# Kernel optimization log

Measured on AMD Instinct MI355X. Metric: run time of the kernel, lower is better.

Reference implementation:

```python
import jax, jax.numpy as jnp
import numpy as np

ALPHA = 16.0
RANK = 64
SCALING = ALPHA / RANK


def setup_inputs() -> dict:
    key = jax.random.key(0)
    k1, k2, k3, k4, k5 = jax.random.split(key, 5)
    B, S, DIN, DOUT = 4, 4096, 4096, 4096
    x = jax.random.normal(k1, (B, S, DIN), dtype=jnp.float32)
    lora_A = jax.random.normal(k2, (RANK, DIN), dtype=jnp.float32) / np.sqrt(DIN)
    lora_B = jax.random.normal(k3, (DOUT, RANK), dtype=jnp.float32)
    lora_A_scale = jax.random.uniform(k4, (RANK,), dtype=jnp.float32, minval=0.5, maxval=1.5)
    lora_B_scale = jax.random.uniform(k5, (DOUT,), dtype=jnp.float32, minval=0.5, maxval=1.5)
    return {"x": x, "lora_A": lora_A, "lora_B": lora_B,
            "lora_A_scale": lora_A_scale, "lora_B_scale": lora_B_scale}


def reference(x, lora_A, lora_B, lora_A_scale, lora_B_scale):
    # INT8 dequant path: quantized.float() * scale.unsqueeze(-1)
    A_dq = lora_A * lora_A_scale[:, None]          # [rank, in]
    B_dq = lora_B * lora_B_scale[:, None]          # [out, rank]
    # x @ A.T -> [B, S, rank]; then @ B.T -> [B, S, out]; final scaling
    h = jnp.einsum('bsi,ri->bsr', x, A_dq)
    out = jnp.einsum('bsr,or->bso', h, B_dq)
    return out * SCALING
```

## Files before the change

kernel.cpp:

```cpp
#include <hip/hip_runtime.h>


#define M_TOTAL 16384
#define DIN     4096
#define DOUT    4096
#define RANK    64

typedef __bf16 bf16_8 __attribute__((ext_vector_type(8)));
typedef __bf16 bf16_4 __attribute__((ext_vector_type(4)));
typedef float  f32x4  __attribute__((ext_vector_type(4)));

__global__ __launch_bounds__(256) void prep_kernel(
    const float* __restrict__ A, const float* __restrict__ Bm,
    const float* __restrict__ sA, const float* __restrict__ sB,
    __bf16* __restrict__ Abf, __bf16* __restrict__ Bbf) {
  int i = (blockIdx.x * 256 + threadIdx.x) * 4;
  float4 a = *(const float4*)(A + i);
  float sa = sA[i >> 12];
  bf16_4 va;
  va[0] = (__bf16)(a.x * sa); va[1] = (__bf16)(a.y * sa);
  va[2] = (__bf16)(a.z * sa); va[3] = (__bf16)(a.w * sa);
  *(bf16_4*)(Abf + i) = va;

  float4 b = *(const float4*)(Bm + i);
  float sb = sB[i >> 6] * 0.25f;
  bf16_4 vb;
  vb[0] = (__bf16)(b.x * sb); vb[1] = (__bf16)(b.y * sb);
  vb[2] = (__bf16)(b.z * sb); vb[3] = (__bf16)(b.w * sb);
  *(bf16_4*)(Bbf + i) = vb;
}

__global__ __launch_bounds__(256, 4) void lora_kernel(
    const float* __restrict__ x, const __bf16* __restrict__ Abf,
    const __bf16* __restrict__ Bbf, float* __restrict__ out) {
  __shared__ alignas(16) float  part[4 * 1024];
  __shared__ alignas(16) __bf16 hs[16 * RANK];

  const int t    = threadIdx.x;
  const int lane = t & 63;
  const int w    = t >> 6;
  const int lr   = lane & 15;
  const int quad = lane >> 4;
  const int mBase = blockIdx.x * 16;

  const float*  xg = x   + (size_t)(mBase + lr) * DIN + w * 1024 + quad * 8;
  const __bf16* ag = Abf + (size_t)lr * DIN           + w * 1024 + quad * 8;

  f32x4 acc0 = {0.f,0.f,0.f,0.f};
  f32x4 acc1 = {0.f,0.f,0.f,0.f};
  f32x4 acc2 = {0.f,0.f,0.f,0.f};
  f32x4 acc3 = {0.f,0.f,0.f,0.f};

  float4 f0 = *(const float4*)(xg);
  float4 f1 = *(const float4*)(xg + 4);
  bf16_8 a0 = *(const bf16_8*)(ag);
  bf16_8 a1 = *(const bf16_8*)(ag + 16 * DIN);
  bf16_8 a2 = *(const bf16_8*)(ag + 32 * DIN);
  bf16_8 a3 = *(const bf16_8*)(ag + 48 * DIN);

  for (int k = 32; k <= 1024; k += 32) {
    float4 g0 = f0, g1 = f1;
    bf16_8 c0 = a0, c1 = a1, c2 = a2, c3 = a3;
    if (k < 1024) {
      f0 = *(const float4*)(xg + k);
      f1 = *(const float4*)(xg + k + 4);
      a0 = *(const bf16_8*)(ag + k);
      a1 = *(const bf16_8*)(ag + k + 16 * DIN);
      a2 = *(const bf16_8*)(ag + k + 32 * DIN);
      a3 = *(const bf16_8*)(ag + k + 48 * DIN);
    }
    bf16_8 xv;
    xv[0] = (__bf16)g0.x; xv[1] = (__bf16)g0.y;
    xv[2] = (__bf16)g0.z; xv[3] = (__bf16)g0.w;
    xv[4] = (__bf16)g1.x; xv[5] = (__bf16)g1.y;
    xv[6] = (__bf16)g1.z; xv[7] = (__bf16)g1.w;
    acc0 = __builtin_amdgcn_mfma_f32_16x16x32_bf16(xv, c0, acc0, 0, 0, 0);
    acc1 = __builtin_amdgcn_mfma_f32_16x16x32_bf16(xv, c1, acc1, 0, 0, 0);
    acc2 = __builtin_amdgcn_mfma_f32_16x16x32_bf16(xv, c2, acc2, 0, 0, 0);
    acc3 = __builtin_amdgcn_mfma_f32_16x16x32_bf16(xv, c3, acc3, 0, 0, 0);
  }

  {
    float* pw = part + w * 1024;
#pragma unroll
    for (int i = 0; i < 4; ++i) {
      pw[(quad * 4 + i) * 64 +      lr] = acc0[i];
      pw[(quad * 4 + i) * 64 + 16 + lr] = acc1[i];
      pw[(quad * 4 + i) * 64 + 32 + lr] = acc2[i];
      pw[(quad * 4 + i) * 64 + 48 + lr] = acc3[i];
    }
  }
  __syncthreads();

  {
    const f32x4* pp = (const f32x4*)part;
    f32x4 s = pp[t] + pp[t + 256] + pp[t + 512] + pp[t + 768];
    bf16_4 hv;
    hv[0] = (__bf16)s[0]; hv[1] = (__bf16)s[1];
    hv[2] = (__bf16)s[2]; hv[3] = (__bf16)s[3];
    ((bf16_4*)hs)[t] = hv;
  }
  __syncthreads();

  bf16_8 hf0 = *(const bf16_8*)&hs[lr * RANK + quad * 8];
  bf16_8 hf1 = *(const bf16_8*)&hs[lr * RANK + 32 + quad * 8];

  const __bf16* bg = Bbf + (size_t)(w * 1024 + lr) * RANK + quad * 8;
  float* og = out + (size_t)(mBase + lr) * DOUT + w * 1024;

#pragma unroll 4
  for (int nt = 0; nt < 64; ++nt) {
    bf16_8 b0 = *(const bf16_8*)(bg + nt * 16 * RANK);
    bf16_8 b1 = *(const bf16_8*)(bg + nt * 16 * RANK + 32);
    f32x4 o = {0.f, 0.f, 0.f, 0.f};
    o = __builtin_amdgcn_mfma_f32_16x16x32_bf16(b0, hf0, o, 0, 0, 0);
    o = __builtin_amdgcn_mfma_f32_16x16x32_bf16(b1, hf1, o, 0, 0, 0);
    *(f32x4*)(og + nt * 16 + quad * 4) = o;
  }
}

extern "C" void kernel_launch(void* const* d_in, const int* in_sizes, int n_in,
                              void* d_out, int out_size, void* d_ws, size_t ws_size,
                              hipStream_t stream) {
  const float* x  = (const float*)d_in[0];
  const float* A  = (const float*)d_in[1];
  const float* Bm = (const float*)d_in[2];
  const float* sA = (const float*)d_in[3];
  const float* sB = (const float*)d_in[4];
  float* out = (float*)d_out;

  __bf16* Abf = (__bf16*)d_ws;
  __bf16* Bbf = Abf + (size_t)RANK * DIN;

  prep_kernel<<<256, 256, 0, stream>>>(A, Bm, sA, sB, Abf, Bbf);
  lora_kernel<<<M_TOTAL / 16, 256, 0, stream>>>(x, Abf, Bbf, out);
}
```

Before: 549.1 us.

## Split fused LoRA kernel into two GEMM kernels with LDS-staged loads and stores

Splits the fused kernel into two: gemm1 streams x through double-buffered LDS using global_load_lds and writes the bf16 intermediate h to workspace, and gemm2 reads h and stages output tiles in swizzled LDS so each row is written to global memory as contiguous wide stores. The aim is more efficient, coalesced traffic on the large x read and the large output write, which dominate this memory-bound workload. The cost is an extra kernel launch, a small h round-trip through memory, and lower occupancy in gemm1.

```diff
diff --git a/kernel.cpp b/kernel.cpp
--- a/kernel.cpp
+++ b/kernel.cpp
@@ -9,6 +9,10 @@
 typedef __bf16 bf16_8 __attribute__((ext_vector_type(8)));
 typedef __bf16 bf16_4 __attribute__((ext_vector_type(4)));
 typedef float  f32x4  __attribute__((ext_vector_type(4)));
+
+#define GLDS16(g, l) __builtin_amdgcn_global_load_lds( \
+    (const __attribute__((address_space(1))) void*)(g), \
+    (__attribute__((address_space(3))) void*)(l), 16, 0, 0)
 
 __global__ __launch_bounds__(256) void prep_kernel(
     const float* __restrict__ A, const float* __restrict__ Bm,
@@ -30,11 +34,94 @@
   *(bf16_4*)(Bbf + i) = vb;
 }
 
-__global__ __launch_bounds__(256, 4) void lora_kernel(
+__global__ __launch_bounds__(256, 2) void gemm1_kernel(
     const float* __restrict__ x, const __bf16* __restrict__ Abf,
-    const __bf16* __restrict__ Bbf, float* __restrict__ out) {
-  __shared__ alignas(16) float  part[4 * 1024];
-  __shared__ alignas(16) __bf16 hs[16 * RANK];
+    __bf16* __restrict__ h) {
+  __shared__ alignas(16) float xs[2][32][256];
+  __shared__ alignas(16) float part[4][16][64];
+
+  const int t    = threadIdx.x;
+  const int lane = t & 63;
+  const int w    = t >> 6;
+  const int lr   = lane & 15;
+  const int quad = lane >> 4;
+  const int mt   = w & 1;
+  const int kh   = w >> 1;
+  const int mBase = blockIdx.x * 32;
+
+  const int swz = w & 1;
+  const float* xsrc = x + (size_t)(mBase + w) * DIN + ((lane ^ swz) << 2);
+
+  const int row = mt * 16 + lr;
+  const int rs  = row & 1;
+
+  f32x4 acc0 = {0.f,0.f,0.f,0.f};
+  f32x4 acc1 = {0.f,0.f,0.f,0.f};
+  f32x4 acc2 = {0.f,0.f,0.f,0.f};
+  f32x4 acc3 = {0.f,0.f,0.f,0.f};
+
+#pragma unroll
+  for (int j = 0; j < 8; ++j)
+    GLDS16(xsrc + (size_t)j * 4 * DIN, &xs[0][w + j * 4][0]);
+  __syncthreads();
+
+  for (int s = 0; s < 16; ++s) {
+    const int buf = s & 1;
+    if (s + 1 < 16) {
+      const float* src = xsrc + (s + 1) * 256;
+#pragma unroll
+      for (int j = 0; j < 8; ++j)
+        GLDS16(src + (size_t)j * 4 * DIN, &xs[buf ^ 1][w + j * 4][0]);
+    }
+    const int k0 = s * 256;
+#pragma unroll
+    for (int ks = 0; ks < 4; ++ks) {
+      const float* px = &xs[buf][row][kh * 128 + ks * 32 + quad * 8];
+      f32x4 lo = *(const f32x4*)(px + (rs ? 4 : 0));
+      f32x4 hi = *(const f32x4*)(px + (rs ? 0 : 4));
+      bf16_8 xv;
+      xv[0]=(__bf16)lo[0]; xv[1]=(__bf16)lo[1]; xv[2]=(__bf16)lo[2]; xv[3]=(__bf16)lo[3];
+      xv[4]=(__bf16)hi[0]; xv[5]=(__bf16)hi[1]; xv[6]=(__bf16)hi[2]; xv[7]=(__bf16)hi[3];
+
+      const __bf16* ap = Abf + (size_t)lr * DIN + k0 + kh * 128 + ks * 32 + quad * 8;
+      bf16_8 a0 = *(const bf16_8*)(ap);
+      bf16_8 a1 = *(const bf16_8*)(ap + 16 * DIN);
+      bf16_8 a2 = *(const bf16_8*)(ap + 32 * DIN);
+      bf16_8 a3 = *(const bf16_8*)(ap + 48 * DIN);
+      acc0 = __builtin_amdgcn_mfma_f32_16x16x32_bf16(xv, a0, acc0, 0, 0, 0);
+      acc1 = __builtin_amdgcn_mfma_f32_16x16x32_bf16(xv, a1, acc1, 0, 0, 0);
+      acc2 = __builtin_amdgcn_mfma_f32_16x16x32_bf16(xv, a2, acc2, 0, 0, 0);
+      acc3 = __builtin_amdgcn_mfma_f32_16x16x32_bf16(xv, a3, acc3, 0, 0, 0);
+    }
+    __syncthreads();
+  }
+
+#pragma unroll
+  for (int i = 0; i < 4; ++i) {
+    part[w][quad * 4 + i][     lr] = acc0[i];
+    part[w][quad * 4 + i][16 + lr] = acc1[i];
+    part[w][quad * 4 + i][32 + lr] = acc2[i];
+    part[w][quad * 4 + i][48 + lr] = acc3[i];
+  }
+  __syncthreads();
+  {
+    int idx = t * 8;
+    int r   = idx >> 6;
+    int c   = idx & 63;
+    int m2  = r >> 4, r16 = r & 15;
+    f32x4 s0 = *(const f32x4*)&part[m2][r16][c]     + *(const f32x4*)&part[m2 + 2][r16][c];
+    f32x4 s1 = *(const f32x4*)&part[m2][r16][c + 4] + *(const f32x4*)&part[m2 + 2][r16][c + 4];
+    bf16_8 hv;
+    hv[0]=(__bf16)s0[0]; hv[1]=(__bf16)s0[1]; hv[2]=(__bf16)s0[2]; hv[3]=(__bf16)s0[3];
+    hv[4]=(__bf16)s1[0]; hv[5]=(__bf16)s1[1]; hv[6]=(__bf16)s1[2]; hv[7]=(__bf16)s1[3];
+    *(bf16_8*)(h + (size_t)(mBase + r) * RANK + c) = hv;
+  }
+}
+
+__global__ __launch_bounds__(256, 4) void gemm2_kernel(
+    const __bf16* __restrict__ h, const __bf16* __restrict__ Bbf,
+    float* __restrict__ out) {
+  __shared__ alignas(16) float os[16][512];
 
   const int t    = threadIdx.x;
   const int lane = t & 63;
@@ -43,79 +130,35 @@
   const int quad = lane >> 4;
   const int mBase = blockIdx.x * 16;
 
-  const float*  xg = x   + (size_t)(mBase + lr) * DIN + w * 1024 + quad * 8;
-  const __bf16* ag = Abf + (size_t)lr * DIN           + w * 1024 + quad * 8;
+  const __bf16* hp = h + (size_t)(mBase + lr) * RANK + quad * 8;
+  bf16_8 hf0 = *(const bf16_8*)(hp);
+  bf16_8 hf1 = *(const bf16_8*)(hp + 32);
 
-  f32x4 acc0 = {0.f,0.f,0.f,0.f};
-  f32x4 acc1 = {0.f,0.f,0.f,0.f};
-  f32x4 acc2 = {0.f,0.f,0.f,0.f};
-  f32x4 acc3 = {0.f,0.f,0.f,0.f};
-
-  float4 f0 = *(const float4*)(xg);
-  float4 f1 = *(const float4*)(xg + 4);
-  bf16_8 a0 = *(const bf16_8*)(ag);
-  bf16_8 a1 = *(const bf16_8*)(ag + 16 * DIN);
-  bf16_8 a2 = *(const bf16_8*)(ag + 32 * DIN);
-  bf16_8 a3 = *(const bf16_8*)(ag + 48 * DIN);
-
-  for (int k = 32; k <= 1024; k += 32) {
-    float4 g0 = f0, g1 = f1;
-    bf16_8 c0 = a0, c1 = a1, c2 = a2, c3 = a3;
-    if (k < 1024) {
-      f0 = *(const float4*)(xg + k);
-      f1 = *(const float4*)(xg + k + 4);
-      a0 = *(const bf16_8*)(ag + k);
-      a1 = *(const bf16_8*)(ag + k + 16 * DIN);
-      a2 = *(const bf16_8*)(ag + k + 32 * DIN);
-      a3 = *(const bf16_8*)(ag + k + 48 * DIN);
+  for (int c = 0; c < 8; ++c) {
+    const int nb = c * 512 + w * 128;
+#pragma unroll
+    for (int tt = 0; tt < 8; ++tt) {
+      const __bf16* bp = Bbf + (size_t)(nb + tt * 16 + lr) * RANK + quad * 8;
+      bf16_8 b0 = *(const bf16_8*)(bp);
+      bf16_8 b1 = *(const bf16_8*)(bp + 32);
+      f32x4 o = {0.f, 0.f, 0.f, 0.f};
+      o = __builtin_amdgcn_mfma_f32_16x16x32_bf16(b0, hf0, o, 0, 0, 0);
+      o = __builtin_amdgcn_mfma_f32_16x16x32_bf16(b1, hf1, o, 0, 0, 0);
+      int colb = (w * 128 + tt * 16 + quad * 4) * 4;
+      int addr = lr * 2048 + (colb ^ ((lr & 7) << 4));
+      *(f32x4*)((char*)os + addr) = o;
     }
-    bf16_8 xv;
-    xv[0] = (__bf16)g0.x; xv[1] = (__bf16)g0.y;
-    xv[2] = (__bf16)g0.z; xv[3] = (__bf16)g0.w;
-    xv[4] = (__bf16)g1.x; xv[5] = (__bf16)g1.y;
-    xv[6] = (__bf16)g1.z; xv[7] = (__bf16)g1.w;
-    acc0 = __builtin_amdgcn_mfma_f32_16x16x32_bf16(xv, c0, acc0, 0, 0, 0);
-    acc1 = __builtin_amdgcn_mfma_f32_16x16x32_bf16(xv, c1, acc1, 0, 0, 0);
-    acc2 = __builtin_amdgcn_mfma_f32_16x16x32_bf16(xv, c2, acc2, 0, 0, 0);
-    acc3 = __builtin_amdgcn_mfma_f32_16x16x32_bf16(xv, c3, acc3, 0, 0, 0);
-  }
-
-  {
-    float* pw = part + w * 1024;
+    __syncthreads();
 #pragma unroll
-    for (int i = 0; i < 4; ++i) {
-      pw[(quad * 4 + i) * 64 +      lr] = acc0[i];
-      pw[(quad * 4 + i) * 64 + 16 + lr] = acc1[i];
-      pw[(quad * 4 + i) * 64 + 32 + lr] = acc2[i];
-      pw[(quad * 4 + i) * 64 + 48 + lr] = acc3[i];
+    for (int r = 0; r < 8; ++r) {
+      int o4   = r * 4096 + t * 16;
+      int rr   = o4 >> 11;
+      int colb = o4 & 2047;
+      int a    = rr * 2048 + (colb ^ ((rr & 7) << 4));
+      f32x4 v  = *(const f32x4*)((const char*)os + a);
+      *(f32x4*)(out + (size_t)(mBase + rr) * DOUT + c * 512 + (colb >> 2)) = v;
     }
-  }
-  __syncthreads();
-
-  {
-    const f32x4* pp = (const f32x4*)part;
-    f32x4 s = pp[t] + pp[t + 256] + pp[t + 512] + pp[t + 768];
-    bf16_4 hv;
-    hv[0] = (__bf16)s[0]; hv[1] = (__bf16)s[1];
-    hv[2] = (__bf16)s[2]; hv[3] = (__bf16)s[3];
-    ((bf16_4*)hs)[t] = hv;
-  }
-  __syncthreads();
-
-  bf16_8 hf0 = *(const bf16_8*)&hs[lr * RANK + quad * 8];
-  bf16_8 hf1 = *(const bf16_8*)&hs[lr * RANK + 32 + quad * 8];
-
-  const __bf16* bg = Bbf + (size_t)(w * 1024 + lr) * RANK + quad * 8;
-  float* og = out + (size_t)(mBase + lr) * DOUT + w * 1024;
-
-#pragma unroll 4
-  for (int nt = 0; nt < 64; ++nt) {
-    bf16_8 b0 = *(const bf16_8*)(bg + nt * 16 * RANK);
-    bf16_8 b1 = *(const bf16_8*)(bg + nt * 16 * RANK + 32);
-    f32x4 o = {0.f, 0.f, 0.f, 0.f};
-    o = __builtin_amdgcn_mfma_f32_16x16x32_bf16(b0, hf0, o, 0, 0, 0);
-    o = __builtin_amdgcn_mfma_f32_16x16x32_bf16(b1, hf1, o, 0, 0, 0);
-    *(f32x4*)(og + nt * 16 + quad * 4) = o;
+    __syncthreads();
   }
 }
 
@@ -131,7 +174,9 @@
 
   __bf16* Abf = (__bf16*)d_ws;
   __bf16* Bbf = Abf + (size_t)RANK * DIN;
+  __bf16* h   = Bbf + (size_t)DOUT * RANK;
 
   prep_kernel<<<256, 256, 0, stream>>>(A, Bm, sA, sB, Abf, Bbf);
-  lora_kernel<<<M_TOTAL / 16, 256, 0, stream>>>(x, Abf, Bbf, out);
+  gemm1_kernel<<<M_TOTAL / 32, 256, 0, stream>>>(x, Abf, h);
+  gemm2_kernel<<<M_TOTAL / 16, 256, 0, stream>>>(h, Bbf, out);
 }
```

New measurement: 501.5 us. 1.09x faster.
